# Performance work log

Measured on AMD Instinct MI355X. Metric: run time of the kernel, lower is better.

## Reference

```python
import jax, jax.numpy as jnp
import numpy as np

SCALE = 100.0  # sharp-softmax temperature from the torch module

def _build_tables():
    # ByteToNibbleFFN: W1 is identity(256) so it is mathematically a no-op; keep W2.
    W2_b2n = np.zeros((256, 32), np.float32)
    bb = np.arange(256)
    W2_b2n[bb, bb >> 4] = 1.0
    W2_b2n[bb, 16 + (bb & 15)] = 1.0
    # NibbleAddWithCarryFFN tables
    W1_add = np.zeros((34, 512), np.float32)
    W2_sum = np.zeros((512, 16), np.float32)
    W2_cout = np.zeros((512, 2), np.float32)
    for a in range(16):
        for b in range(16):
            for c in range(2):
                idx = a * 32 + b * 2 + c
                W1_add[a, idx] = 1.0
                W1_add[16 + b, idx] = 1.0
                W1_add[32 + c, idx] = 1.0
                t = a + b + c
                W2_sum[idx, t & 15] = 1.0
                W2_cout[idx, 1 if t > 15 else 0] = 1.0
    # NibbleToByteFFN tables
    W1_n2b = np.zeros((32, 256), np.float32)
    W2_n2b = np.zeros((256, 256), np.float32)
    for h in range(16):
        for l in range(16):
            addr = h * 16 + l
            W1_n2b[h, addr] = 1.0
            W1_n2b[16 + l, addr] = 1.0
            W2_n2b[addr, (h << 4) | l] = 1.0
    return tuple(jnp.asarray(t) for t in (W2_b2n, W1_add, W2_sum, W2_cout, W1_n2b, W2_n2b))

W2_B2N, W1_ADD, W2_SUM, W2_COUT, W1_N2B, W2_N2B = _build_tables()

def _b2n(x):
    # byte [.,256] -> (high [.,16], low [.,16]); W1=eye(256) omitted (identity)
    out = x @ W2_B2N
    return out[..., :16], out[..., 16:]

def _nib_add(a, b, cin):
    combined = jnp.concatenate([a, b, cin], axis=-1)           # [.,34]
    address = jax.nn.softmax(combined @ W1_ADD * SCALE, axis=-1)  # [.,512]
    return address @ W2_SUM, address @ W2_COUT

def _n2b(high, low):
    combined = jnp.concatenate([high, low], axis=-1)           # [.,32]
    address = jax.nn.softmax(combined @ W1_N2B * SCALE, axis=-1)  # [.,256]
    return address @ W2_N2B

def setup_inputs() -> dict:
    key = jax.random.key(0)
    k1, k2 = jax.random.split(key)
    B = 32768
    a = jax.random.uniform(k1, (B, 4, 256), dtype=jnp.float32)
    b = jax.random.uniform(k2, (B, 4, 256), dtype=jnp.float32)
    return {"a": a, "b": b}

def reference(a, b):
    # NeuralALU.add: ripple-carry add over 4 bytes, 2 nibble adds per byte
    B = a.shape[0]
    carry = jnp.zeros((B, 2), a.dtype).at[:, 0].set(1.0)  # carry_zero one-hot
    out_bytes = []
    for i in range(4):  # fixed structural loop over bytes (carry dependence)
        ah, al = _b2n(a[:, i])
        bh, bl = _b2n(b[:, i])
        sl, carry = _nib_add(al, bl, carry)
        sh, carry = _nib_add(ah, bh, carry)
        out_bytes.append(_n2b(sh, sl))
    return jnp.stack(out_bytes, axis=1)  # [B,4,256]
```

## Files before the change

### kernel.cpp

```cpp
#include <hip/hip_runtime.h>

#define NIB_SCALE 100.0f

__device__ __forceinline__ float bcast16(float v, int srcLane) {
    return __shfl(v, srcLane, 16);
}

__device__ __forceinline__ float rmax16(float v) {
    #pragma unroll
    for (int m = 1; m < 16; m <<= 1) v = fmaxf(v, __shfl_xor(v, m, 16));
    return v;
}

__device__ __forceinline__ float rsum16(float v) {
    #pragma unroll
    for (int m = 1; m < 16; m <<= 1) v += __shfl_xor(v, m, 16);
    return v;
}

__device__ __forceinline__ float transposeReduce16(const float x[16], int k) {
    float w[16];
    #pragma unroll
    for (int e = 0; e < 16; ++e) w[e] = x[e];
    #pragma unroll
    for (int d = 0; d < 4; ++d) {
        const int m = 1 << d;
        const int bit = (k >> d) & 1;
        const int n = 16 >> (d + 1);
        #pragma unroll
        for (int j = 0; j < n; ++j) {
            float keep = bit ? w[2 * j + 1] : w[2 * j];
            float send = bit ? w[2 * j]     : w[2 * j + 1];
            float recv = __shfl_xor(send, m, 16);
            w[j] = keep + recv;
        }
    }
    return w[0];
}

__device__ __forceinline__ float softmax16(float v) {
    float m = rmax16(v);
    float e = __expf(NIB_SCALE * (v - m));
    float s = rsum16(e);
    return e / s;
}

__global__ __launch_bounds__(256) void nalu_kernel(const float* __restrict__ A,
                                                   const float* __restrict__ B,
                                                   float* __restrict__ O,
                                                   int nrows) {
    const int tid = threadIdx.x;
    const int k = tid & 15;
    const int row = blockIdx.x * 16 + (tid >> 4);
    if (row >= nrows) return;
    const long base = (long)row * 1024;

    float pc0 = 1.0f, pc1 = 0.0f;

    #pragma unroll
    for (int byte = 0; byte < 4; ++byte) {
        const float* pa = A + base + byte * 256;
        const float* pb = B + base + byte * 256;

        float xa[16], xb[16];
        #pragma unroll
        for (int e = 0; e < 16; ++e) xa[e] = pa[16 * e + k];
        #pragma unroll
        for (int e = 0; e < 16; ++e) xb[e] = pb[16 * e + k];

        float al = 0.f, bl = 0.f;
        #pragma unroll
        for (int e = 0; e < 16; ++e) al += xa[e];
        #pragma unroll
        for (int e = 0; e < 16; ++e) bl += xb[e];
        float ah = transposeReduce16(xa, k);
        float bh = transposeReduce16(xb, k);

        float pal = softmax16(al);
        float pbl = softmax16(bl);
        float pah = softmax16(ah);
        float pbh = softmax16(bh);

        float rl = 0.f, rh = 0.f;
        #pragma unroll
        for (int a = 0; a < 16; ++a) {
            float pa_l = bcast16(pal, a);
            float pa_h = bcast16(pah, a);
            float pb_l = bcast16(pbl, (k - a) & 15);
            float pb_h = bcast16(pbh, (k - a) & 15);
            rl = fmaf(pa_l, pb_l, rl);
            rh = fmaf(pa_h, pb_h, rh);
        }

        float Tl = pbl, Th = pbh;
        #pragma unroll
        for (int d = 1; d < 16; d <<= 1) {
            float tl = __shfl_down(Tl, d, 16);
            float th = __shfl_down(Th, d, 16);
            if (k + d < 16) { Tl += tl; Th += th; }
        }
        float T15l = bcast16(Tl, 15 - k);
        float T15h = bcast16(Th, 15 - k);
        float B15l = bcast16(pbl, 15 - k);
        float B15h = bcast16(pbh, 15 - k);
        float ov15l = rsum16(pal * T15l);
        float c15l  = rsum16(pal * B15l);
        float ov15h = rsum16(pah * T15h);
        float c15h  = rsum16(pah * B15h);
        float ov16l = ov15l - c15l;
        float ov16h = ov15h - c15h;

        float rlm1  = bcast16(rl, (k - 1) & 15);
        float slow  = pc0 * rl + pc1 * rlm1;
        float coutl = pc0 * ov16l + pc1 * ov15l;

        float e1  = __expf(NIB_SCALE * (1.0f - 2.0f * coutl));
        float qc1 = 1.0f / (1.0f + e1);
        float qc0 = 1.0f - qc1;

        float rhm1  = bcast16(rh, (k - 1) & 15);
        float shigh = qc0 * rh + qc1 * rhm1;
        float couth = qc0 * ov16h + qc1 * ov15h;

        float e2 = __expf(NIB_SCALE * (1.0f - 2.0f * couth));
        pc1 = 1.0f / (1.0f + e2);
        pc0 = 1.0f - pc1;

        float psl = softmax16(slow);
        float psh = softmax16(shigh);

        float* po = O + base + byte * 256;
        float l0 = bcast16(psl, 4 * (k & 3) + 0);
        float l1 = bcast16(psl, 4 * (k & 3) + 1);
        float l2 = bcast16(psl, 4 * (k & 3) + 2);
        float l3 = bcast16(psl, 4 * (k & 3) + 3);
        #pragma unroll
        for (int c = 0; c < 4; ++c) {
            float hs = bcast16(psh, 4 * c + (k >> 2));
            float4 o4 = make_float4(hs * l0, hs * l1, hs * l2, hs * l3);
            *(float4*)(po + 64 * c + 4 * k) = o4;
        }
    }
}

extern "C" void kernel_launch(void* const* d_in, const int* in_sizes, int n_in,
                              void* d_out, int out_size, void* d_ws, size_t ws_size,
                              hipStream_t stream) {
    const float* A = (const float*)d_in[0];
    const float* B = (const float*)d_in[1];
    float* O = (float*)d_out;
    int nrows = in_sizes[0] / 1024;
    int grid = (nrows + 15) / 16;
    nalu_kernel<<<grid, 256, 0, stream>>>(A, B, O, nrows);
}
```

Before: 327.8 us.

## Replace shuffles with DPP row ops and LDS staging, load nibble sums directly

Swaps the 16-lane __shfl-based reductions, broadcasts and scan for DPP row_shr/row_ror/row_mirror intrinsics. The high-nibble sums now come from a second set of contiguous float4 loads per lane instead of a shuffle transpose-reduce. The nibble convolution gathers rotated pa values through DPP and reads pb from an LDS row. The output outer product is staged through LDS so each lane writes 16 contiguous floats. This removes many ds_bpermute shuffles at the cost of loading the inputs twice, which relies on cache hits, and of less coalesced stores. The LDS staging has no barrier, so it depends on each 16-lane group sitting inside a single wavefront.

```diff
diff --git a/kernel.cpp b/kernel.cpp
--- a/kernel.cpp
+++ b/kernel.cpp
@@ -2,56 +2,71 @@
 
 #define NIB_SCALE 100.0f
 
-__device__ __forceinline__ float bcast16(float v, int srcLane) {
-    return __shfl(v, srcLane, 16);
+template<int CTRL>
+__device__ __forceinline__ float fdpp(float x) {
+    return __int_as_float(__builtin_amdgcn_update_dpp(
+        0, __float_as_int(x), CTRL, 0xF, 0xF, true));
 }
 
-__device__ __forceinline__ float rmax16(float v) {
-    #pragma unroll
-    for (int m = 1; m < 16; m <<= 1) v = fmaxf(v, __shfl_xor(v, m, 16));
+__device__ __forceinline__ float rsum16d(float v) {
+    v += fdpp<0x121>(v);
+    v += fdpp<0x122>(v);
+    v += fdpp<0x124>(v);
+    v += fdpp<0x128>(v);
+    return v;
+}
+__device__ __forceinline__ float rmax16d(float v) {
+    v = fmaxf(v, fdpp<0x121>(v));
+    v = fmaxf(v, fdpp<0x122>(v));
+    v = fmaxf(v, fdpp<0x124>(v));
+    v = fmaxf(v, fdpp<0x128>(v));
+    return v;
+}
+__device__ __forceinline__ float scan16d(float v) {
+    v += fdpp<0x111>(v);
+    v += fdpp<0x112>(v);
+    v += fdpp<0x114>(v);
+    v += fdpp<0x118>(v);
     return v;
 }
 
-__device__ __forceinline__ float rsum16(float v) {
-    #pragma unroll
-    for (int m = 1; m < 16; m <<= 1) v += __shfl_xor(v, m, 16);
-    return v;
+__device__ __forceinline__ float softmax16d(float v) {
+    float m = rmax16d(v);
+    float e = expf(NIB_SCALE * (v - m));
+    float s = rsum16d(e);
+    return e / s;
 }
 
-__device__ __forceinline__ float transposeReduce16(const float x[16], int k) {
-    float w[16];
-    #pragma unroll
-    for (int e = 0; e < 16; ++e) w[e] = x[e];
-    #pragma unroll
-    for (int d = 0; d < 4; ++d) {
-        const int m = 1 << d;
-        const int bit = (k >> d) & 1;
-        const int n = 16 >> (d + 1);
-        #pragma unroll
-        for (int j = 0; j < n; ++j) {
-            float keep = bit ? w[2 * j + 1] : w[2 * j];
-            float send = bit ? w[2 * j]     : w[2 * j + 1];
-            float recv = __shfl_xor(send, m, 16);
-            w[j] = keep + recv;
-        }
-    }
-    return w[0];
-}
-
-__device__ __forceinline__ float softmax16(float v) {
-    float m = rmax16(v);
-    float e = __expf(NIB_SCALE * (v - m));
-    float s = rsum16(e);
-    return e / s;
-}
+#define GATHER_ROT(dst, src)            \
+    dst[0]  = (src);                    \
+    dst[1]  = fdpp<0x121>(src);         \
+    dst[2]  = fdpp<0x122>(src);         \
+    dst[3]  = fdpp<0x123>(src);         \
+    dst[4]  = fdpp<0x124>(src);         \
+    dst[5]  = fdpp<0x125>(src);         \
+    dst[6]  = fdpp<0x126>(src);         \
+    dst[7]  = fdpp<0x127>(src);         \
+    dst[8]  = fdpp<0x128>(src);         \
+    dst[9]  = fdpp<0x129>(src);         \
+    dst[10] = fdpp<0x12A>(src);         \
+    dst[11] = fdpp<0x12B>(src);         \
+    dst[12] = fdpp<0x12C>(src);         \
+    dst[13] = fdpp<0x12D>(src);         \
+    dst[14] = fdpp<0x12E>(src);         \
+    dst[15] = fdpp<0x12F>(src);
 
 __global__ __launch_bounds__(256) void nalu_kernel(const float* __restrict__ A,
                                                    const float* __restrict__ B,
                                                    float* __restrict__ O,
                                                    int nrows) {
+    __shared__ __align__(16) float sQL[16][16];
+    __shared__ __align__(16) float sQH[16][16];
+    __shared__ __align__(16) float sPSL[16][16];
+
     const int tid = threadIdx.x;
     const int k = tid & 15;
-    const int row = blockIdx.x * 16 + (tid >> 4);
+    const int g = tid >> 4;
+    const int row = blockIdx.x * 16 + g;
     if (row >= nrows) return;
     const long base = (long)row * 1024;
 
@@ -62,83 +77,99 @@
         const float* pa = A + base + byte * 256;
         const float* pb = B + base + byte * 256;
 
-        float xa[16], xb[16];
+        float sa[16], sb[16];
         #pragma unroll
-        for (int e = 0; e < 16; ++e) xa[e] = pa[16 * e + k];
+        for (int e = 0; e < 16; ++e) sa[e] = pa[16 * e + k];
         #pragma unroll
-        for (int e = 0; e < 16; ++e) xb[e] = pb[16 * e + k];
+        for (int e = 0; e < 16; ++e) sb[e] = pb[16 * e + k];
+        const float4* pa4 = (const float4*)(pa + 16 * k);
+        const float4* pb4 = (const float4*)(pb + 16 * k);
+        float4 ra0 = pa4[0], ra1 = pa4[1], ra2 = pa4[2], ra3 = pa4[3];
+        float4 rb0 = pb4[0], rb1 = pb4[1], rb2 = pb4[2], rb3 = pb4[3];
 
         float al = 0.f, bl = 0.f;
         #pragma unroll
-        for (int e = 0; e < 16; ++e) al += xa[e];
+        for (int e = 0; e < 16; ++e) al += sa[e];
         #pragma unroll
-        for (int e = 0; e < 16; ++e) bl += xb[e];
-        float ah = transposeReduce16(xa, k);
-        float bh = transposeReduce16(xb, k);
+        for (int e = 0; e < 16; ++e) bl += sb[e];
+        float4 rat = make_float4(ra0.x + ra1.x + ra2.x + ra3.x,
+                                 ra0.y + ra1.y + ra2.y + ra3.y,
+                                 ra0.z + ra1.z + ra2.z + ra3.z,
+                                 ra0.w + ra1.w + ra2.w + ra3.w);
+        float4 rbt = make_float4(rb0.x + rb1.x + rb2.x + rb3.x,
+                                 rb0.y + rb1.y + rb2.y + rb3.y,
+                                 rb0.z + rb1.z + rb2.z + rb3.z,
+                                 rb0.w + rb1.w + rb2.w + rb3.w);
+        float ah = (rat.x + rat.y) + (rat.z + rat.w);
+        float bh = (rbt.x + rbt.y) + (rbt.z + rbt.w);
 
-        float pal = softmax16(al);
-        float pbl = softmax16(bl);
-        float pah = softmax16(ah);
-        float pbh = softmax16(bh);
+        float pal = softmax16d(al);
+        float pbl = softmax16d(bl);
+        float pah = softmax16d(ah);
+        float pbh = softmax16d(bh);
 
-        float rl = 0.f, rh = 0.f;
-        #pragma unroll
-        for (int a = 0; a < 16; ++a) {
-            float pa_l = bcast16(pal, a);
-            float pa_h = bcast16(pah, a);
-            float pb_l = bcast16(pbl, (k - a) & 15);
-            float pb_h = bcast16(pbh, (k - a) & 15);
-            rl = fmaf(pa_l, pb_l, rl);
-            rh = fmaf(pa_h, pb_h, rh);
-        }
+        sQL[g][k] = pbl;
+        sQH[g][k] = pbh;
 
-        float Tl = pbl, Th = pbh;
-        #pragma unroll
-        for (int d = 1; d < 16; d <<= 1) {
-            float tl = __shfl_down(Tl, d, 16);
-            float th = __shfl_down(Th, d, 16);
-            if (k + d < 16) { Tl += tl; Th += th; }
-        }
-        float T15l = bcast16(Tl, 15 - k);
-        float T15h = bcast16(Th, 15 - k);
-        float B15l = bcast16(pbl, 15 - k);
-        float B15h = bcast16(pbh, 15 - k);
-        float ov15l = rsum16(pal * T15l);
-        float c15l  = rsum16(pal * B15l);
-        float ov15h = rsum16(pah * T15h);
-        float c15h  = rsum16(pah * B15h);
+        float mirl = fdpp<0x140>(pbl);
+        float mirh = fdpp<0x140>(pbh);
+        float T15l = scan16d(mirl);
+        float T15h = scan16d(mirh);
+        float ov15l = rsum16d(pal * T15l);
+        float c15l  = rsum16d(pal * mirl);
+        float ov15h = rsum16d(pah * T15h);
+        float c15h  = rsum16d(pah * mirh);
         float ov16l = ov15l - c15l;
         float ov16h = ov15h - c15h;
 
-        float rlm1  = bcast16(rl, (k - 1) & 15);
+        float QL[16], QH[16];
+        *(float4*)&QL[0]  = *(const float4*)&sQL[g][0];
+        *(float4*)&QL[4]  = *(const float4*)&sQL[g][4];
+        *(float4*)&QL[8]  = *(const float4*)&sQL[g][8];
+        *(float4*)&QL[12] = *(const float4*)&sQL[g][12];
+        *(float4*)&QH[0]  = *(const float4*)&sQH[g][0];
+        *(float4*)&QH[4]  = *(const float4*)&sQH[g][4];
+        *(float4*)&QH[8]  = *(const float4*)&sQH[g][8];
+        *(float4*)&QH[12] = *(const float4*)&sQH[g][12];
+
+        float GL[16], GH[16];
+        GATHER_ROT(GL, pal)
+        GATHER_ROT(GH, pah)
+        float rl = 0.f, rh = 0.f;
+        #pragma unroll
+        for (int j = 0; j < 16; ++j) {
+            rl = fmaf(GL[j], QL[j], rl);
+            rh = fmaf(GH[j], QH[j], rh);
+        }
+
+        float rlm1  = fdpp<0x121>(rl);
         float slow  = pc0 * rl + pc1 * rlm1;
         float coutl = pc0 * ov16l + pc1 * ov15l;
-
-        float e1  = __expf(NIB_SCALE * (1.0f - 2.0f * coutl));
-        float qc1 = 1.0f / (1.0f + e1);
+        float qc1 = 1.0f / (1.0f + expf(NIB_SCALE * (1.0f - 2.0f * coutl)));
         float qc0 = 1.0f - qc1;
 
-        float rhm1  = bcast16(rh, (k - 1) & 15);
+        float rhm1  = fdpp<0x121>(rh);
         float shigh = qc0 * rh + qc1 * rhm1;
         float couth = qc0 * ov16h + qc1 * ov15h;
-
-        float e2 = __expf(NIB_SCALE * (1.0f - 2.0f * couth));
-        pc1 = 1.0f / (1.0f + e2);
+        pc1 = 1.0f / (1.0f + expf(NIB_SCALE * (1.0f - 2.0f * couth)));
         pc0 = 1.0f - pc1;
 
-        float psl = softmax16(slow);
-        float psh = softmax16(shigh);
+        float psl = softmax16d(slow);
+        float psh = softmax16d(shigh);
 
-        float* po = O + base + byte * 256;
-        float l0 = bcast16(psl, 4 * (k & 3) + 0);
-        float l1 = bcast16(psl, 4 * (k & 3) + 1);
-        float l2 = bcast16(psl, 4 * (k & 3) + 2);
-        float l3 = bcast16(psl, 4 * (k & 3) + 3);
+        sPSL[g][k] = psl;
+        float PSL[16];
+        *(float4*)&PSL[0]  = *(const float4*)&sPSL[g][0];
+        *(float4*)&PSL[4]  = *(const float4*)&sPSL[g][4];
+        *(float4*)&PSL[8]  = *(const float4*)&sPSL[g][8];
+        *(float4*)&PSL[12] = *(const float4*)&sPSL[g][12];
+
+        float* po = O + base + byte * 256 + 16 * k;
         #pragma unroll
         for (int c = 0; c < 4; ++c) {
-            float hs = bcast16(psh, 4 * c + (k >> 2));
-            float4 o4 = make_float4(hs * l0, hs * l1, hs * l2, hs * l3);
-            *(float4*)(po + 64 * c + 4 * k) = o4;
+            float4 o4 = make_float4(psh * PSL[4 * c + 0], psh * PSL[4 * c + 1],
+                                    psh * PSL[4 * c + 2], psh * PSL[4 * c + 3]);
+            *(float4*)(po + 4 * c) = o4;
         }
     }
 }
```

Result: no change. 332.9 us (+1.6%).
